# Kernel tuning notes

Hardware: AMD Instinct MI355X
Metric: run time of the kernel (lower is better)

## Reference

```python
import jax, jax.numpy as jnp
import numpy as np

B, Hc, Wc, C, NH, SR, WS = 4, 64, 64, 256, 8, 2, 4
N = Hc * Wc


def _window_partition(x, ws, H, W):
    # x: (B, h, N, d) -> (B*h*nWin, ws*ws, d)
    Bb, h, _, d = x.shape
    x = x.reshape(Bb * h, H // ws, ws, W // ws, ws, d)
    x = x.transpose(0, 1, 3, 2, 4, 5)
    return x.reshape(-1, ws * ws, d)


def _window_reverse(win, ws, H, W, head):
    nwin = (H // ws) * (W // ws)
    Bh = win.shape[0] // nwin
    x = win.reshape(Bh, H // ws, W // ws, ws, ws, -1).transpose(0, 1, 3, 2, 4, 5).reshape(Bh, H, W, -1)
    Bb = Bh // head
    x = x.reshape(Bb, head, H, W, -1).transpose(0, 2, 3, 1, 4)  # heads interleave into channels
    return x.reshape(Bb, H * W, -1)


def _layernorm(x, w, b):
    m = x.mean(-1, keepdims=True)
    v = x.var(-1, keepdims=True)
    return (x - m) / jnp.sqrt(v + 1e-5) * w + b


def setup_inputs() -> dict:
    key = jax.random.key(0)
    ks = jax.random.split(key, 16)
    lin = lambda k, i, o: 0.02 * jax.random.normal(k, (i, o), jnp.float32)
    inp = {
        'x': jax.random.normal(ks[0], (B, N, C), jnp.float32),
        'q1_w': lin(ks[1], C, C // 2), 'q1_b': jnp.zeros((C // 2,), jnp.float32),
        'kv1_w': lin(ks[2], C, C), 'kv1_b': jnp.zeros((C,), jnp.float32),
        'q2_w': lin(ks[3], C, C // 2), 'q2_b': jnp.zeros((C // 2,), jnp.float32),
        'kv2_w': lin(ks[4], C, C), 'kv2_b': jnp.zeros((C,), jnp.float32),
        'lepe_w': lin(ks[5], C, C), 'lepe_b': jnp.zeros((C,), jnp.float32),
        'lepe_conv_w': jnp.sqrt(2.0 / 9.0) * jax.random.normal(ks[6], (C, 1, 3, 3), jnp.float32),
        'lepe_conv_b': jnp.zeros((C,), jnp.float32),
        'sr_w': jnp.sqrt(2.0 / (SR * SR * C)) * jax.random.normal(ks[7], (C, C, SR, SR), jnp.float32),
        'sr_b': jnp.zeros((C,), jnp.float32),
        'norm_w': jnp.ones((C,), jnp.float32), 'norm_b': jnp.zeros((C,), jnp.float32),
        'proj_w': lin(ks[8], C, C), 'proj_b': jnp.zeros((C,), jnp.float32),
        'H': Hc, 'W': Wc,
    }
    return inp


def reference(x, q1_w, q1_b, kv1_w, kv1_b, q2_w, q2_b, kv2_w, kv2_b,
              lepe_w, lepe_b, lepe_conv_w, lepe_conv_b, sr_w, sr_b,
              norm_w, norm_b, proj_w, proj_b, H, W):
    Bb, Nn, Cc = x.shape
    h2 = NH // 2
    d = Cc // NH
    sr = sr_w.shape[-1]
    scale = d ** -0.5
    ws = WS

    # lepe: linear -> depthwise 3x3 conv
    l = (x @ lepe_w + lepe_b).transpose(0, 2, 1).reshape(Bb, Cc, H, W)
    l = jax.lax.conv_general_dilated(l, lepe_conv_w, (1, 1), ((1, 1), (1, 1)),
                                     dimension_numbers=('NCHW', 'OIHW', 'NCHW'),
                                     feature_group_count=Cc) + lepe_conv_b[None, :, None, None]
    lepe = l.reshape(Bb, Cc, Nn).transpose(0, 2, 1)

    # branch 1: spatial-reduction global attention
    q1 = (x @ q1_w + q1_b).reshape(Bb, Nn, h2, d).transpose(0, 2, 1, 3)
    x_img = x.transpose(0, 2, 1).reshape(Bb, Cc, H, W)
    xs = jax.lax.conv_general_dilated(x_img, sr_w, (sr, sr), 'VALID',
                                      dimension_numbers=('NCHW', 'OIHW', 'NCHW')) + sr_b[None, :, None, None]
    N1 = (H // sr) * (W // sr)
    xs = xs.reshape(Bb, Cc, N1).transpose(0, 2, 1)
    xs = jax.nn.gelu(_layernorm(xs, norm_w, norm_b), approximate=False)
    kv1 = (xs @ kv1_w + kv1_b).reshape(Bb, N1, 2, h2, d).transpose(2, 0, 3, 1, 4)
    k1, v1 = kv1[0], kv1[1]
    attn1 = jax.nn.softmax(jnp.einsum('bhnd,bhmd->bhnm', q1, k1) * scale, axis=-1)
    x1 = jnp.einsum('bhnm,bhmd->bnhd', attn1, v1).reshape(Bb, Nn, Cc // 2)
    g = jax.lax.stop_gradient(attn1).mean(1).mean(1).reshape(Bb, H // sr, W // sr)
    g = jnp.repeat(jnp.repeat(g, sr, axis=1), sr, axis=2)  # nearest upsample to (B,H,W)

    # branch 2: Swin-style windowed attention (window 4)
    q2 = (x @ q2_w + q2_b).reshape(Bb, Nn, h2, d).transpose(0, 2, 1, 3)
    kv2 = (x @ kv2_w + kv2_b).reshape(Bb, Nn, 2, h2, d).transpose(2, 0, 3, 1, 4)
    k2, v2 = kv2[0], kv2[1]
    q2w = _window_partition(q2, ws, H, W)
    k2w = _window_partition(k2, ws, H, W)
    v2w = _window_partition(v2, ws, H, W)
    attn2 = jax.nn.softmax(jnp.einsum('wnd,wmd->wnm', q2w, k2w) * scale, axis=-1)
    x2 = jnp.einsum('wnm,wmd->wnd', attn2, v2w)
    x2 = _window_reverse(x2, ws, H, W, h2)
    nwin = (H // ws) * (W // ws)
    lm = jax.lax.stop_gradient(attn2).reshape(Bb, h2, nwin, ws * ws, ws * ws).mean(1).mean(2)
    lm = lm.reshape(Bb, H // ws, W // ws, ws, ws).transpose(0, 1, 3, 2, 4).reshape(Bb, H, W)

    out = jnp.concatenate([x1, x2], axis=-1)
    p = (out + lepe) @ proj_w + proj_b
    out = p + p  # proj_drop is identity at p=0.0, so x = drop(p) + p = 2p

    mask = lm + g
    mask1 = mask.reshape(Bb, H * W)
    mask2 = mask.transpose(0, 2, 1).reshape(Bb, H * W)
    return out, mask1, mask2
```

## Files before the change

### kernel.cpp

```cpp
#include <hip/hip_runtime.h>
#include <hip/hip_bf16.h>
#include <math.h>

typedef __hip_bfloat16 bf16;
typedef __attribute__((ext_vector_type(8))) short bf16x8;
typedef __attribute__((ext_vector_type(4))) short bf16x4;
typedef __attribute__((ext_vector_type(4))) float f32x4;

__device__ __forceinline__ float b2f(bf16 v) { return __bfloat162float(v); }
__device__ __forceinline__ bf16  f2b(float v) { return __float2bfloat16(v); }
__device__ __forceinline__ float s2f(short v) { return __uint_as_float(((unsigned)(unsigned short)v) << 16); }

__global__ void detect_dtype(const void* x, int* flag)
{
    __shared__ int cnt;
    if (threadIdx.x == 0) cnt = 0;
    __syncthreads();
    const unsigned* w = (const unsigned*)x;
    int sane = 0;
    for (int i = threadIdx.x; i < 2048; i += 256) {
        unsigned lo = (w[i] & 0xFFFFu) << 16;
        float v = __uint_as_float(lo);
        float a = fabsf(v);
        if (v == 0.f || (a > 1e-8f && a < 1e4f)) sane++;
    }
    atomicAdd(&cnt, sane);
    __syncthreads();
    if (threadIdx.x == 0) *flag = (cnt < 1640) ? 1 : 0;
}

__global__ void convert_x4(const void* __restrict__ src, bf16* __restrict__ dst,
                           const int* __restrict__ flag)
{
    int i = blockIdx.x * 256 + threadIdx.x;
    bf16 tmp[4];
    if (*flag) {
        float4 v = ((const float4*)src)[i];
        tmp[0] = f2b(v.x); tmp[1] = f2b(v.y); tmp[2] = f2b(v.z); tmp[3] = f2b(v.w);
        *(bf16x4*)&dst[i * 4] = *(bf16x4*)tmp;
    } else {
        ((bf16x4*)dst)[i] = ((const bf16x4*)src)[i];
    }
}

struct PackArgs { const void* src[10]; bf16* dst[10]; int n[10]; };
__global__ void pack_small(PackArgs a, const int* __restrict__ flag)
{
    int bi = blockIdx.x;
    int n = a.n[bi];
    const void* s = a.src[bi];
    bf16* d = a.dst[bi];
    for (int i = threadIdx.x; i < n; i += 256)
        d[i] = (*flag) ? f2b(((const float*)s)[i]) : f2b(s2f(((const short*)s)[i]));
}

struct WTArgs { const void* src[6]; bf16* dst[6]; int N[6]; int blkoff[7]; };
__global__ void convert_wT_multi(WTArgs a, const int* __restrict__ flag)
{
    int blk = blockIdx.x;
    int ti = 0;
    while (blk >= a.blkoff[ti + 1]) ++ti;
    int o = (blk - a.blkoff[ti]) * 256 + threadIdx.x;
    int n = o >> 8, k = o & 255;
    int N = a.N[ti];
    float v = (*flag) ? ((const float*)a.src[ti])[k * N + n]
                      : s2f(((const short*)a.src[ti])[k * N + n]);
    a.dst[ti][o] = f2b(v);
}

__global__ void convert_srwT(const void* __restrict__ src, bf16* __restrict__ dst,
                             const int* __restrict__ flag)
{
    int o = blockIdx.x * 256 + threadIdx.x;
    int co = o >> 10, kg = o & 1023;
    int e = kg >> 8, ci = kg & 255;
    int si = co * 1024 + ci * 4 + e;
    float v = (*flag) ? ((const float*)src)[si] : s2f(((const short*)src)[si]);
    dst[o] = f2b(v);
}

__global__ void convert_dwT(const void* __restrict__ src, bf16* __restrict__ dst,
                            const int* __restrict__ flag)
{
    int o = blockIdx.x * 256 + threadIdx.x;
    if (o >= 2304) return;
    int k = o >> 8, c = o & 255;
    float v = (*flag) ? ((const float*)src)[c * 9 + k] : s2f(((const short*)src)[c * 9 + k]);
    dst[o] = f2b(v);
}

__global__ __launch_bounds__(256) void gemm_qkv(
    const bf16* __restrict__ A, const bf16* __restrict__ WT, const bf16* __restrict__ bias,
    bf16* __restrict__ Cl, bf16* __restrict__ Cq1, bf16* __restrict__ Cq2, bf16* __restrict__ Ckv2)
{
    __shared__ bf16 As[64][40];
    __shared__ bf16 Bs[64][40];
    int t = threadIdx.x;
    int m0 = blockIdx.x * 64, n0g = blockIdx.y * 64;
    int w = t >> 6, l = t & 63, lane16 = l & 15, quad = l >> 4;
    int sr = t >> 2, sc = (t & 3) * 8;
    f32x4 acc[4] = {};
    for (int k0 = 0; k0 < 256; k0 += 32) {
        *(bf16x8*)&As[sr][sc] = *(const bf16x8*)&A[(size_t)(m0 + sr) * 256 + k0 + sc];
        *(bf16x8*)&Bs[sr][sc] = *(const bf16x8*)&WT[(size_t)(n0g + sr) * 256 + k0 + sc];
        __syncthreads();
        bf16x8 a = *(const bf16x8*)&As[w * 16 + lane16][quad * 8];
        #pragma unroll
        for (int ct = 0; ct < 4; ++ct) {
            bf16x8 b = *(const bf16x8*)&Bs[ct * 16 + lane16][quad * 8];
            acc[ct] = __builtin_amdgcn_mfma_f32_16x16x32_bf16(a, b, acc[ct], 0, 0, 0);
        }
        __syncthreads();
    }
    bf16* C; int base, N;
    if (n0g < 256)      { C = Cl;   base = 0;   N = 256; }
    else if (n0g < 384) { C = Cq1;  base = 256; N = 128; }
    else if (n0g < 512) { C = Cq2;  base = 384; N = 128; }
    else                { C = Ckv2; base = 512; N = 256; }
    #pragma unroll
    for (int ct = 0; ct < 4; ++ct) {
        int colg = n0g + ct * 16 + lane16;
        float bv = b2f(bias[colg]);
        #pragma unroll
        for (int r = 0; r < 4; ++r) {
            int row = m0 + w * 16 + quad * 4 + r;
            C[(size_t)row * N + (colg - base)] = f2b(acc[ct][r] + bv);
        }
    }
}

__global__ __launch_bounds__(256) void gemm_sr_mfma(
    const bf16* __restrict__ x, const bf16* __restrict__ WT,
    const bf16* __restrict__ bias, bf16* __restrict__ C)
{
    __shared__ bf16 As[64][40];
    __shared__ bf16 Bs[64][40];
    int t = threadIdx.x;
    int m0 = blockIdx.x * 64, n0 = blockIdx.y * 64;
    int w = t >> 6, l = t & 63, lane16 = l & 15, quad = l >> 4;
    int sr = t >> 2, sc = (t & 3) * 8;
    int brow = m0 + sr;
    int b = brow >> 10, p = brow & 1023;
    int pi = p >> 5, pj = p & 31;
    f32x4 acc[4] = {};
    for (int k0 = 0; k0 < 1024; k0 += 32) {
        int kg = k0 + sc;
        int e = kg >> 8, ci = kg & 255;
        int di = e >> 1, dj = e & 1;
        int n = (2 * pi + di) * 64 + 2 * pj + dj;
        *(bf16x8*)&As[sr][sc] = *(const bf16x8*)&x[(size_t)((b << 12) + n) * 256 + ci];
        *(bf16x8*)&Bs[sr][sc] = *(const bf16x8*)&WT[(size_t)(n0 + sr) * 1024 + kg];
        __syncthreads();
        bf16x8 a = *(const bf16x8*)&As[w * 16 + lane16][quad * 8];
        #pragma unroll
        for (int ct = 0; ct < 4; ++ct) {
            bf16x8 bb = *(const bf16x8*)&Bs[ct * 16 + lane16][quad * 8];
            acc[ct] = __builtin_amdgcn_mfma_f32_16x16x32_bf16(a, bb, acc[ct], 0, 0, 0);
        }
        __syncthreads();
    }
    #pragma unroll
    for (int ct = 0; ct < 4; ++ct) {
        int col = n0 + ct * 16 + lane16;
        float bv = b2f(bias[col]);
        #pragma unroll
        for (int r = 0; r < 4; ++r) {
            int row = m0 + w * 16 + quad * 4 + r;
            C[(size_t)row * 256 + col] = f2b(acc[ct][r] + bv);
        }
    }
}

__global__ __launch_bounds__(256) void gemm_kv1(
    const bf16* __restrict__ A, const bf16* __restrict__ WT, const bf16* __restrict__ bias,
    bf16* __restrict__ k1, bf16* __restrict__ v1T)
{
    __shared__ bf16 As[64][40];
    __shared__ bf16 Bs[64][40];
    int t = threadIdx.x;
    int m0 = blockIdx.x * 64, n0 = blockIdx.y * 64;
    int w = t >> 6, l = t & 63, lane16 = l & 15, quad = l >> 4;
    int sr = t >> 2, sc = (t & 3) * 8;
    f32x4 acc[4] = {};
    for (int k0 = 0; k0 < 256; k0 += 32) {
        *(bf16x8*)&As[sr][sc] = *(const bf16x8*)&A[(size_t)(m0 + sr) * 256 + k0 + sc];
        *(bf16x8*)&Bs[sr][sc] = *(const bf16x8*)&WT[(size_t)(n0 + sr) * 256 + k0 + sc];
        __syncthreads();
        bf16x8 a = *(const bf16x8*)&As[w * 16 + lane16][quad * 8];
        #pragma unroll
        for (int ct = 0; ct < 4; ++ct) {
            bf16x8 b = *(const bf16x8*)&Bs[ct * 16 + lane16][quad * 8];
            acc[ct] = __builtin_amdgcn_mfma_f32_16x16x32_bf16(a, b, acc[ct], 0, 0, 0);
        }
        __syncthreads();
    }
    #pragma unroll
    for (int ct = 0; ct < 4; ++ct) {
        int col = n0 + ct * 16 + lane16;
        float bv = b2f(bias[col]);
        #pragma unroll
        for (int r = 0; r < 4; ++r) {
            int row = m0 + w * 16 + quad * 4 + r;
            float val = acc[ct][r] + bv;
            int bb = row >> 10, key = row & 1023;
            if (col < 128) {
                k1[(size_t)row * 128 + col] = f2b(val);
            } else {
                int h = (col - 128) >> 5, ch = (col - 128) & 31;
                v1T[(size_t)((bb * 4 + h) * 32 + ch) * 1024 + key] = f2b(val);
            }
        }
    }
}

__global__ __launch_bounds__(256) void gemm_proj_mfma(
    const bf16* __restrict__ A, const bf16* __restrict__ A2,
    const bf16* __restrict__ WT, const bf16* __restrict__ bias,
    void* __restrict__ dout, const int* __restrict__ flag)
{
    __shared__ bf16 As[64][40];
    __shared__ bf16 Bs[64][40];
    int t = threadIdx.x;
    int m0 = blockIdx.x * 64, n0 = blockIdx.y * 64;
    int w = t >> 6, l = t & 63, lane16 = l & 15, quad = l >> 4;
    int sr = t >> 2, sc = (t & 3) * 8;
    f32x4 acc[4] = {};
    for (int k0 = 0; k0 < 256; k0 += 32) {
        const bf16* pa = &A[(size_t)(m0 + sr) * 256 + k0 + sc];
        const bf16* pb = &A2[(size_t)(m0 + sr) * 256 + k0 + sc];
        bf16 tmp[8];
        #pragma unroll
        for (int j = 0; j < 8; ++j) tmp[j] = f2b(b2f(pa[j]) + b2f(pb[j]));
        *(bf16x8*)&As[sr][sc] = *(bf16x8*)tmp;
        *(bf16x8*)&Bs[sr][sc] = *(const bf16x8*)&WT[(size_t)(n0 + sr) * 256 + k0 + sc];
        __syncthreads();
        bf16x8 a = *(const bf16x8*)&As[w * 16 + lane16][quad * 8];
        #pragma unroll
        for (int ct = 0; ct < 4; ++ct) {
            bf16x8 b = *(const bf16x8*)&Bs[ct * 16 + lane16][quad * 8];
            acc[ct] = __builtin_amdgcn_mfma_f32_16x16x32_bf16(a, b, acc[ct], 0, 0, 0);
        }
        __syncthreads();
    }
    #pragma unroll
    for (int ct = 0; ct < 4; ++ct) {
        int col = n0 + ct * 16 + lane16;
        float bv = b2f(bias[col]);
        #pragma unroll
        for (int r = 0; r < 4; ++r) {
            int row = m0 + w * 16 + quad * 4 + r;
            float rv = (acc[ct][r] + bv) * 2.f;
            size_t o = (size_t)row * 256 + col;
            if (*flag) ((float*)dout)[o] = rv;
            else       ((bf16*)dout)[o] = f2b(rv);
        }
    }
}

__global__ __launch_bounds__(256) void dwconv3v(
    const bf16* __restrict__ lin, const bf16* __restrict__ dwT,
    const bf16* __restrict__ bias, bf16* __restrict__ out)
{
    int tid = blockIdx.x * 256 + threadIdx.x;
    int c0 = (tid & 31) * 8;
    int n = (tid >> 5) & 4095;
    int b = tid >> 17;
    int i = n >> 6, j = n & 63;
    float acc[8];
    bf16x8 bv = *(const bf16x8*)&bias[c0];
    #pragma unroll
    for (int q = 0; q < 8; ++q) acc[q] = s2f(bv[q]);
    #pragma unroll
    for (int di = 0; di < 3; ++di) {
        int ii = i + di - 1;
        if (ii < 0 || ii > 63) continue;
        #pragma unroll
        for (int dj = 0; dj < 3; ++dj) {
            int jj = j + dj - 1;
            if (jj < 0 || jj > 63) continue;
            bf16x8 xv = *(const bf16x8*)&lin[(size_t)((b << 12) + ii * 64 + jj) * 256 + c0];
            bf16x8 wv = *(const bf16x8*)&dwT[(di * 3 + dj) * 256 + c0];
            #pragma unroll
            for (int q = 0; q < 8; ++q) acc[q] += s2f(xv[q]) * s2f(wv[q]);
        }
    }
    bf16 ov[8];
    #pragma unroll
    for (int q = 0; q < 8; ++q) ov[q] = f2b(acc[q]);
    *(bf16x8*)&out[(size_t)((b << 12) + n) * 256 + c0] = *(bf16x8*)ov;
}

__global__ __launch_bounds__(256) void ln_gelu_w(
    const bf16* __restrict__ xin, const bf16* __restrict__ nw,
    const bf16* __restrict__ nb, bf16* __restrict__ xout)
{
    int w = threadIdx.x >> 6, lane = threadIdx.x & 63;
    int r = blockIdx.x * 4 + w;
    bf16x4 xv = *(const bf16x4*)&xin[(size_t)r * 256 + lane * 4];
    float v[4];
    #pragma unroll
    for (int j = 0; j < 4; ++j) v[j] = s2f(xv[j]);
    float s = v[0] + v[1] + v[2] + v[3];
    #pragma unroll
    for (int o = 1; o <= 32; o <<= 1) s += __shfl_xor(s, o);
    float mean = s * (1.f / 256.f);
    float ss = 0.f;
    #pragma unroll
    for (int j = 0; j < 4; ++j) { float d = v[j] - mean; ss += d * d; }
    #pragma unroll
    for (int o = 1; o <= 32; o <<= 1) ss += __shfl_xor(ss, o);
    float inv = rsqrtf(ss * (1.f / 256.f) + 1e-5f);
    bf16x4 wv = *(const bf16x4*)&nw[lane * 4];
    bf16x4 bv = *(const bf16x4*)&nb[lane * 4];
    bf16 ov[4];
    #pragma unroll
    for (int j = 0; j < 4; ++j) {
        float y = (v[j] - mean) * inv * s2f(wv[j]) + s2f(bv[j]);
        ov[j] = f2b(0.5f * y * (1.f + erff(y * 0.70710678118654752f)));
    }
    *(bf16x4*)&xout[(size_t)r * 256 + lane * 4] = *(bf16x4*)ov;
}

__global__ __launch_bounds__(256) void attn1_mfma2(
    const bf16* __restrict__ q1, const bf16* __restrict__ k1,
    const bf16* __restrict__ v1T, bf16* __restrict__ attn_out, float* __restrict__ g)
{
    __shared__ bf16 Kt[64][40];
    __shared__ bf16 Vt[32][68];
    __shared__ bf16 Pw[4][16][72];
    __shared__ float gp[1024];

    int t = threadIdx.x;
    int blk = blockIdx.x;
    int qc = blk & 63, h = (blk >> 6) & 3, b = blk >> 8;
    int n0 = qc * 64;
    int w = t >> 6, l = t & 63, lane16 = l & 15, quad = l >> 4;
    int sr = t >> 2, sc = (t & 3) * 8;
    const float scale = 0.17677669529663687f;

    bf16x8 qa = *(const bf16x8*)&q1[(size_t)(b * 4096 + n0 + 16 * w + lane16) * 128 + 32 * h + quad * 8];
    const bf16* Kbase = k1 + (size_t)b * 1024 * 128 + 32 * h;
    const bf16* Vbase = v1T + (size_t)((b * 4 + h) * 32) * 1024;

    for (int i = t; i < 1024; i += 256) gp[i] = 0.f;

    float lacc[4] = {0.f, 0.f, 0.f, 0.f};
    for (int kt = 0; kt < 16; ++kt) {
        *(bf16x8*)&Kt[sr][sc] = *(const bf16x8*)&Kbase[(size_t)(kt * 64 + sr) * 128 + sc];
        __syncthreads();
        #pragma unroll
        for (int st = 0; st < 4; ++st) {
            bf16x8 kb = *(const bf16x8*)&Kt[st * 16 + lane16][quad * 8];
            f32x4 z = {0.f, 0.f, 0.f, 0.f};
            f32x4 s = __builtin_amdgcn_mfma_f32_16x16x32_bf16(qa, kb, z, 0, 0, 0);
            #pragma unroll
            for (int r = 0; r < 4; ++r) lacc[r] += __expf(s[r] * scale);
        }
        __syncthreads();
    }
    float rl[4];
    #pragma unroll
    for (int r = 0; r < 4; ++r) {
        float v = lacc[r];
        v += __shfl_xor(v, 1); v += __shfl_xor(v, 2);
        v += __shfl_xor(v, 4); v += __shfl_xor(v, 8);
        rl[r] = 1.f / v;
    }

    f32x4 oacc0 = {}, oacc1 = {};
    int vrow = t >> 3, vcol = (t & 7) * 8;
    for (int kt = 0; kt < 16; ++kt) {
        *(bf16x8*)&Kt[sr][sc] = *(const bf16x8*)&Kbase[(size_t)(kt * 64 + sr) * 128 + sc];
        *(bf16x8*)&Vt[vrow][vcol] = *(const bf16x8*)&Vbase[(size_t)vrow * 1024 + kt * 64 + vcol];
        __syncthreads();
        #pragma unroll
        for (int st = 0; st < 4; ++st) {
            bf16x8 kb = *(const bf16x8*)&Kt[st * 16 + lane16][quad * 8];
            f32x4 z = {0.f, 0.f, 0.f, 0.f};
            f32x4 s = __builtin_amdgcn_mfma_f32_16x16x32_bf16(qa, kb, z, 0, 0, 0);
            float cs = 0.f;
            #pragma unroll
            for (int r = 0; r < 4; ++r) {
                float p = __expf(s[r] * scale) * rl[r];
                Pw[w][quad * 4 + r][st * 16 + lane16] = f2b(p);
                cs += p;
            }
            cs += __shfl_xor(cs, 16);
            cs += __shfl_xor(cs, 32);
            if (quad == 0) atomicAdd(&gp[kt * 64 + st * 16 + lane16], cs);
        }
        #pragma unroll
        for (int kh = 0; kh < 2; ++kh) {
            bf16x8 pa = *(const bf16x8*)&Pw[w][lane16][kh * 32 + quad * 8];
            bf16x8 vb0 = *(const bf16x8*)&Vt[lane16][kh * 32 + quad * 8];
            bf16x8 vb1 = *(const bf16x8*)&Vt[16 + lane16][kh * 32 + quad * 8];
            oacc0 = __builtin_amdgcn_mfma_f32_16x16x32_bf16(pa, vb0, oacc0, 0, 0, 0);
            oacc1 = __builtin_amdgcn_mfma_f32_16x16x32_bf16(pa, vb1, oacc1, 0, 0, 0);
        }
        __syncthreads();
    }

    #pragma unroll
    for (int r = 0; r < 4; ++r) {
        size_t ro = (size_t)(b * 4096 + n0 + 16 * w + quad * 4 + r) * 256 + 32 * h;
        attn_out[ro + lane16] = f2b(oacc0[r]);
        attn_out[ro + 16 + lane16] = f2b(oacc1[r]);
    }
    for (int i = t; i < 1024; i += 256)
        atomicAdd(&g[(b << 10) + i], gp[i] * (1.f / 16384.f));
}

__global__ __launch_bounds__(64) void attn2_vec(
    const bf16* __restrict__ q2, const bf16* __restrict__ kv2,
    bf16* __restrict__ attn_out, float* __restrict__ lm)
{
    __shared__ float P2[64][17];
    int t = threadIdx.x;
    int blk = blockIdx.x;
    int b = blk >> 8, win = blk & 255;
    int wi = win >> 4, wj = win & 15;
    int h = t >> 4, qi = t & 15;
    int nq = (wi * 4 + (qi >> 2)) * 64 + wj * 4 + (qi & 3);

    float qv[32];
    {
        const bf16* qp = q2 + (size_t)(b * 4096 + nq) * 128 + h * 32;
        #pragma unroll
        for (int g8 = 0; g8 < 4; ++g8) {
            bf16x8 v = *(const bf16x8*)&qp[g8 * 8];
            #pragma unroll
            for (int j = 0; j < 8; ++j) qv[g8 * 8 + j] = s2f(v[j]) * 0.17677669529663687f;
        }
    }
    float s[16];
    float mx = -1e30f;
    #pragma unroll
    for (int k = 0; k < 16; ++k) {
        int nk = (wi * 4 + (k >> 2)) * 64 + wj * 4 + (k & 3);
        const bf16* kp = kv2 + (size_t)(b * 4096 + nk) * 256 + h * 32;
        float ss = 0.f;
        #pragma unroll
        for (int g8 = 0; g8 < 4; ++g8) {
            bf16x8 v = *(const bf16x8*)&kp[g8 * 8];
            #pragma unroll
            for (int j = 0; j < 8; ++j) ss += qv[g8 * 8 + j] * s2f(v[j]);
        }
        s[k] = ss;
        mx = fmaxf(mx, ss);
    }
    float lsum = 0.f;
    #pragma unroll
    for (int k = 0; k < 16; ++k) { s[k] = __expf(s[k] - mx); lsum += s[k]; }
    float rl = 1.f / lsum;
    #pragma unroll
    for (int k = 0; k < 16; ++k) s[k] *= rl;

    float o[32];
    #pragma unroll
    for (int d = 0; d < 32; ++d) o[d] = 0.f;
    #pragma unroll
    for (int k = 0; k < 16; ++k) {
        int nk = (wi * 4 + (k >> 2)) * 64 + wj * 4 + (k & 3);
        const bf16* vp = kv2 + (size_t)(b * 4096 + nk) * 256 + 128 + h * 32;
        float p = s[k];
        #pragma unroll
        for (int g8 = 0; g8 < 4; ++g8) {
            bf16x8 v = *(const bf16x8*)&vp[g8 * 8];
            #pragma unroll
            for (int j = 0; j < 8; ++j) o[g8 * 8 + j] += p * s2f(v[j]);
        }
    }
    {
        bf16* op = attn_out + (size_t)(b * 4096 + nq) * 256 + 128 + h * 32;
        #pragma unroll
        for (int g8 = 0; g8 < 4; ++g8) {
            bf16 ov[8];
            #pragma unroll
            for (int j = 0; j < 8; ++j) ov[j] = f2b(o[g8 * 8 + j]);
            *(bf16x8*)&op[g8 * 8] = *(bf16x8*)ov;
        }
    }

    #pragma unroll
    for (int k = 0; k < 16; ++k) P2[t][k] = s[k];
    __syncthreads();
    if (t < 16) {
        float cs = 0.f;
        for (int qq = 0; qq < 64; ++qq) cs += P2[qq][t];
        int nk = (wi * 4 + (t >> 2)) * 64 + wj * 4 + (t & 3);
        lm[(b << 12) + nk] = cs * (1.f / 64.f);
    }
}

__global__ void mask_combine(const float* __restrict__ lm, const float* __restrict__ g,
                             void* __restrict__ dout, const int* __restrict__ flag)
{
    int tid = blockIdx.x * 256 + threadIdx.x;
    int b = tid >> 12, n = tid & 4095;
    int i = n >> 6, j = n & 63;
    float v = lm[tid] + g[(b << 10) + (i >> 1) * 32 + (j >> 1)];
    size_t o1 = (size_t)4194304 + (b << 12) + i * 64 + j;
    size_t o2 = (size_t)4194304 + 16384 + (b << 12) + j * 64 + i;
    if (*flag) { ((float*)dout)[o1] = v; ((float*)dout)[o2] = v; }
    else       { ((bf16*)dout)[o1] = f2b(v); ((bf16*)dout)[o2] = f2b(v); }
}

extern "C" void kernel_launch(void* const* d_in, const int* in_sizes, int n_in,
                              void* d_out, int out_size, void* d_ws, size_t ws_size,
                              hipStream_t stream)
{
    char* ws = (char*)d_ws;
    size_t off = 0;
    auto alloc = [&](size_t bytes) {
        void* p = ws + off;
        off += (bytes + 255) & ~(size_t)255;
        return p;
    };
    bf16* cx       = (bf16*)alloc((size_t)4194304 * 2);
    bf16* lepe_lin = (bf16*)alloc((size_t)4194304 * 2);
    bf16* attn_out = lepe_lin;
    bf16* lepe     = (bf16*)alloc((size_t)4194304 * 2);
    bf16* q1buf    = (bf16*)alloc((size_t)2097152 * 2);
    bf16* q2buf    = (bf16*)alloc((size_t)2097152 * 2);
    bf16* kv2buf   = (bf16*)alloc((size_t)4194304 * 2);
    bf16* xs_pre   = (bf16*)alloc((size_t)1048576 * 2);
    bf16* k1buf    = xs_pre;
    bf16* v1Tbuf   = xs_pre + 524288;
    bf16* xs       = (bf16*)alloc((size_t)1048576 * 2);
    bf16* wTqkv    = (bf16*)alloc((size_t)196608 * 2);
    bf16* kv1_wT   = (bf16*)alloc(65536 * 2);
    bf16* proj_wT  = (bf16*)alloc(65536 * 2);
    bf16* sr_wT    = (bf16*)alloc(262144 * 2);
    bf16* dwT      = (bf16*)alloc(2304 * 2);
    bf16* bcat     = (bf16*)alloc(768 * 2);
    bf16* ckv1b    = (bf16*)alloc(256 * 2);
    bf16* csrb     = (bf16*)alloc(256 * 2);
    bf16* cnw      = (bf16*)alloc(256 * 2);
    bf16* cnb      = (bf16*)alloc(256 * 2);
    bf16* cpb      = (bf16*)alloc(256 * 2);
    bf16* clcb     = (bf16*)alloc(256 * 2);
    float* gbuf    = (float*)alloc(4096 * 4);
    float* lmbuf   = (float*)alloc(16384 * 4);
    int*   flag    = (int*)alloc(256);

    detect_dtype<<<1, 256, 0, stream>>>(d_in[0], flag);

    convert_x4<<<4096, 256, 0, stream>>>(d_in[0], cx, flag);

    PackArgs pa;
    pa.src[0] = d_in[10]; pa.dst[0] = bcat;       pa.n[0] = 256;
    pa.src[1] = d_in[2];  pa.dst[1] = bcat + 256; pa.n[1] = 128;
    pa.src[2] = d_in[6];  pa.dst[2] = bcat + 384; pa.n[2] = 128;
    pa.src[3] = d_in[8];  pa.dst[3] = bcat + 512; pa.n[3] = 256;
    pa.src[4] = d_in[4];  pa.dst[4] = ckv1b;      pa.n[4] = 256;
    pa.src[5] = d_in[14]; pa.dst[5] = csrb;       pa.n[5] = 256;
    pa.src[6] = d_in[15]; pa.dst[6] = cnw;        pa.n[6] = 256;
    pa.src[7] = d_in[16]; pa.dst[7] = cnb;        pa.n[7] = 256;
    pa.src[8] = d_in[18]; pa.dst[8] = cpb;        pa.n[8] = 256;
    pa.src[9] = d_in[12]; pa.dst[9] = clcb;       pa.n[9] = 256;
    pack_small<<<10, 256, 0, stream>>>(pa, flag);

    WTArgs wa;
    wa.src[0] = d_in[9];  wa.dst[0] = wTqkv;             wa.N[0] = 256;
    wa.src[1] = d_in[1];  wa.dst[1] = wTqkv + 256 * 256; wa.N[1] = 128;
    wa.src[2] = d_in[5];  wa.dst[2] = wTqkv + 384 * 256; wa.N[2] = 128;
    wa.src[3] = d_in[7];  wa.dst[3] = wTqkv + 512 * 256; wa.N[3] = 256;
    wa.src[4] = d_in[3];  wa.dst[4] = kv1_wT;            wa.N[4] = 256;
    wa.src[5] = d_in[17]; wa.dst[5] = proj_wT;           wa.N[5] = 256;
    int bo[7] = {0, 256, 384, 512, 768, 1024, 1280};
    for (int i = 0; i < 7; ++i) wa.blkoff[i] = bo[i];
    convert_wT_multi<<<1280, 256, 0, stream>>>(wa, flag);

    convert_srwT<<<1024, 256, 0, stream>>>(d_in[13], sr_wT, flag);
    convert_dwT<<<9, 256, 0, stream>>>(d_in[11], dwT, flag);

    hipMemsetAsync(gbuf, 0, 4096 * 4, stream);

    gemm_qkv<<<dim3(256, 12), 256, 0, stream>>>(cx, wTqkv, bcat, lepe_lin, q1buf, q2buf, kv2buf);
    gemm_sr_mfma<<<dim3(64, 4), 256, 0, stream>>>(cx, sr_wT, csrb, xs_pre);
    ln_gelu_w<<<1024, 256, 0, stream>>>(xs_pre, cnw, cnb, xs);
    gemm_kv1<<<dim3(64, 4), 256, 0, stream>>>(xs, kv1_wT, ckv1b, k1buf, v1Tbuf);
    dwconv3v<<<2048, 256, 0, stream>>>(lepe_lin, dwT, clcb, lepe);
    attn1_mfma2<<<1024, 256, 0, stream>>>(q1buf, k1buf, v1Tbuf, attn_out, gbuf);
    attn2_vec<<<1024, 64, 0, stream>>>(q2buf, kv2buf, attn_out, lmbuf);
    gemm_proj_mfma<<<dim3(256, 4), 256, 0, stream>>>(attn_out, lepe, proj_wT, cpb, d_out, flag);
    mask_combine<<<64, 256, 0, stream>>>(lmbuf, gbuf, d_out, flag);
}
```

Measured before the change: 277.7 us.

## Use 128x128 GEMM tiles and restructure attention-1 into single-pass transposed PV

The QKV and projection GEMMs move from 64x64 to 128x128 block tiles, with each wave computing a 4x4 grid of MFMA tiles. This gives more register-level reuse per LDS load at the cost of more accumulator registers and fewer blocks. The global attention kernel now accumulates unnormalised P·V in the first pass with transposed MFMAs and normalises at the end, so the second pass only computes the mask column sums. It also drops the shared K/V staging and per-tile block barriers in favour of direct global loads into registers, which risks less coalesced access.

```diff
diff --git a/kernel.cpp b/kernel.cpp
--- a/kernel.cpp
+++ b/kernel.cpp
@@ -89,43 +89,110 @@
     dst[o] = f2b(v);
 }
 
-__global__ __launch_bounds__(256) void gemm_qkv(
+__global__ __launch_bounds__(256) void gemm_qkv128(
     const bf16* __restrict__ A, const bf16* __restrict__ WT, const bf16* __restrict__ bias,
     bf16* __restrict__ Cl, bf16* __restrict__ Cq1, bf16* __restrict__ Cq2, bf16* __restrict__ Ckv2)
 {
-    __shared__ bf16 As[64][40];
-    __shared__ bf16 Bs[64][40];
+    __shared__ bf16 As[128][40];
+    __shared__ bf16 Bs[128][40];
     int t = threadIdx.x;
-    int m0 = blockIdx.x * 64, n0g = blockIdx.y * 64;
+    int m0 = blockIdx.x * 128, ybase = blockIdx.y * 128;
     int w = t >> 6, l = t & 63, lane16 = l & 15, quad = l >> 4;
-    int sr = t >> 2, sc = (t & 3) * 8;
-    f32x4 acc[4] = {};
+    int wr = w >> 1, wc = w & 1;
+    int sr = t >> 1, sc = (t & 1) * 16;
+    f32x4 acc[4][4] = {};
     for (int k0 = 0; k0 < 256; k0 += 32) {
-        *(bf16x8*)&As[sr][sc] = *(const bf16x8*)&A[(size_t)(m0 + sr) * 256 + k0 + sc];
-        *(bf16x8*)&Bs[sr][sc] = *(const bf16x8*)&WT[(size_t)(n0g + sr) * 256 + k0 + sc];
-        __syncthreads();
-        bf16x8 a = *(const bf16x8*)&As[w * 16 + lane16][quad * 8];
-        #pragma unroll
-        for (int ct = 0; ct < 4; ++ct) {
-            bf16x8 b = *(const bf16x8*)&Bs[ct * 16 + lane16][quad * 8];
-            acc[ct] = __builtin_amdgcn_mfma_f32_16x16x32_bf16(a, b, acc[ct], 0, 0, 0);
-        }
-        __syncthreads();
-    }
-    bf16* C; int base, N;
-    if (n0g < 256)      { C = Cl;   base = 0;   N = 256; }
-    else if (n0g < 384) { C = Cq1;  base = 256; N = 128; }
-    else if (n0g < 512) { C = Cq2;  base = 384; N = 128; }
-    else                { C = Ckv2; base = 512; N = 256; }
-    #pragma unroll
-    for (int ct = 0; ct < 4; ++ct) {
-        int colg = n0g + ct * 16 + lane16;
-        float bv = b2f(bias[colg]);
-        #pragma unroll
-        for (int r = 0; r < 4; ++r) {
-            int row = m0 + w * 16 + quad * 4 + r;
-            C[(size_t)row * N + (colg - base)] = f2b(acc[ct][r] + bv);
-        }
+        *(bf16x8*)&As[sr][sc]     = *(const bf16x8*)&A[(size_t)(m0 + sr) * 256 + k0 + sc];
+        *(bf16x8*)&As[sr][sc + 8] = *(const bf16x8*)&A[(size_t)(m0 + sr) * 256 + k0 + sc + 8];
+        *(bf16x8*)&Bs[sr][sc]     = *(const bf16x8*)&WT[(size_t)(ybase + sr) * 256 + k0 + sc];
+        *(bf16x8*)&Bs[sr][sc + 8] = *(const bf16x8*)&WT[(size_t)(ybase + sr) * 256 + k0 + sc + 8];
+        __syncthreads();
+        bf16x8 a[4], b[4];
+        #pragma unroll
+        for (int i = 0; i < 4; ++i) {
+            a[i] = *(const bf16x8*)&As[wr * 64 + i * 16 + lane16][quad * 8];
+            b[i] = *(const bf16x8*)&Bs[wc * 64 + i * 16 + lane16][quad * 8];
+        }
+        #pragma unroll
+        for (int i = 0; i < 4; ++i)
+            #pragma unroll
+            for (int j = 0; j < 4; ++j)
+                acc[i][j] = __builtin_amdgcn_mfma_f32_16x16x32_bf16(a[i], b[j], acc[i][j], 0, 0, 0);
+        __syncthreads();
+    }
+    bf16* C; int N, cbase;
+    if (ybase < 256)      { C = Cl;   N = 256; cbase = ybase; }
+    else if (ybase < 384) { C = Cq1;  N = 128; cbase = ybase - 256; }
+    else if (ybase < 512) { C = Cq2;  N = 128; cbase = ybase - 384; }
+    else                  { C = Ckv2; N = 256; cbase = ybase - 512; }
+    #pragma unroll
+    for (int j = 0; j < 4; ++j) {
+        int gcol = ybase + wc * 64 + j * 16 + lane16;
+        float bv = b2f(bias[gcol]);
+        int col = cbase + wc * 64 + j * 16 + lane16;
+        #pragma unroll
+        for (int i = 0; i < 4; ++i)
+            #pragma unroll
+            for (int r = 0; r < 4; ++r) {
+                int row = m0 + wr * 64 + i * 16 + quad * 4 + r;
+                C[(size_t)row * N + col] = f2b(acc[i][j][r] + bv);
+            }
+    }
+}
+
+__global__ __launch_bounds__(256) void gemm_proj128(
+    const bf16* __restrict__ A, const bf16* __restrict__ A2,
+    const bf16* __restrict__ WT, const bf16* __restrict__ bias,
+    void* __restrict__ dout, const int* __restrict__ flag)
+{
+    __shared__ bf16 As[128][40];
+    __shared__ bf16 Bs[128][40];
+    int t = threadIdx.x;
+    int m0 = blockIdx.x * 128, n0 = blockIdx.y * 128;
+    int w = t >> 6, l = t & 63, lane16 = l & 15, quad = l >> 4;
+    int wr = w >> 1, wc = w & 1;
+    int sr = t >> 1, sc = (t & 1) * 16;
+    f32x4 acc[4][4] = {};
+    for (int k0 = 0; k0 < 256; k0 += 32) {
+        #pragma unroll
+        for (int hh = 0; hh < 2; ++hh) {
+            bf16x8 va = *(const bf16x8*)&A[(size_t)(m0 + sr) * 256 + k0 + sc + hh * 8];
+            bf16x8 vb = *(const bf16x8*)&A2[(size_t)(m0 + sr) * 256 + k0 + sc + hh * 8];
+            bf16 tmp[8];
+            #pragma unroll
+            for (int q = 0; q < 8; ++q) tmp[q] = f2b(s2f(va[q]) + s2f(vb[q]));
+            *(bf16x8*)&As[sr][sc + hh * 8] = *(bf16x8*)tmp;
+        }
+        *(bf16x8*)&Bs[sr][sc]     = *(const bf16x8*)&WT[(size_t)(n0 + sr) * 256 + k0 + sc];
+        *(bf16x8*)&Bs[sr][sc + 8] = *(const bf16x8*)&WT[(size_t)(n0 + sr) * 256 + k0 + sc + 8];
+        __syncthreads();
+        bf16x8 a[4], b[4];
+        #pragma unroll
+        for (int i = 0; i < 4; ++i) {
+            a[i] = *(const bf16x8*)&As[wr * 64 + i * 16 + lane16][quad * 8];
+            b[i] = *(const bf16x8*)&Bs[wc * 64 + i * 16 + lane16][quad * 8];
+        }
+        #pragma unroll
+        for (int i = 0; i < 4; ++i)
+            #pragma unroll
+            for (int j = 0; j < 4; ++j)
+                acc[i][j] = __builtin_amdgcn_mfma_f32_16x16x32_bf16(a[i], b[j], acc[i][j], 0, 0, 0);
+        __syncthreads();
+    }
+    #pragma unroll
+    for (int j = 0; j < 4; ++j) {
+        int col = n0 + wc * 64 + j * 16 + lane16;
+        float bv = b2f(bias[col]);
+        #pragma unroll
+        for (int i = 0; i < 4; ++i)
+            #pragma unroll
+            for (int r = 0; r < 4; ++r) {
+                int row = m0 + wr * 64 + i * 16 + quad * 4 + r;
+                float rv = (acc[i][j][r] + bv) * 2.f;
+                size_t o = (size_t)row * 256 + col;
+                if (*flag) ((float*)dout)[o] = rv;
+                else       ((bf16*)dout)[o] = f2b(rv);
+            }
     }
 }
 
@@ -213,50 +280,6 @@
     }
 }
 
-__global__ __launch_bounds__(256) void gemm_proj_mfma(
-    const bf16* __restrict__ A, const bf16* __restrict__ A2,
-    const bf16* __restrict__ WT, const bf16* __restrict__ bias,
-    void* __restrict__ dout, const int* __restrict__ flag)
-{
-    __shared__ bf16 As[64][40];
-    __shared__ bf16 Bs[64][40];
-    int t = threadIdx.x;
-    int m0 = blockIdx.x * 64, n0 = blockIdx.y * 64;
-    int w = t >> 6, l = t & 63, lane16 = l & 15, quad = l >> 4;
-    int sr = t >> 2, sc = (t & 3) * 8;
-    f32x4 acc[4] = {};
-    for (int k0 = 0; k0 < 256; k0 += 32) {
-        const bf16* pa = &A[(size_t)(m0 + sr) * 256 + k0 + sc];
-        const bf16* pb = &A2[(size_t)(m0 + sr) * 256 + k0 + sc];
-        bf16 tmp[8];
-        #pragma unroll
-        for (int j = 0; j < 8; ++j) tmp[j] = f2b(b2f(pa[j]) + b2f(pb[j]));
-        *(bf16x8*)&As[sr][sc] = *(bf16x8*)tmp;
-        *(bf16x8*)&Bs[sr][sc] = *(const bf16x8*)&WT[(size_t)(n0 + sr) * 256 + k0 + sc];
-        __syncthreads();
-        bf16x8 a = *(const bf16x8*)&As[w * 16 + lane16][quad * 8];
-        #pragma unroll
-        for (int ct = 0; ct < 4; ++ct) {
-            bf16x8 b = *(const bf16x8*)&Bs[ct * 16 + lane16][quad * 8];
-            acc[ct] = __builtin_amdgcn_mfma_f32_16x16x32_bf16(a, b, acc[ct], 0, 0, 0);
-        }
-        __syncthreads();
-    }
-    #pragma unroll
-    for (int ct = 0; ct < 4; ++ct) {
-        int col = n0 + ct * 16 + lane16;
-        float bv = b2f(bias[col]);
-        #pragma unroll
-        for (int r = 0; r < 4; ++r) {
-            int row = m0 + w * 16 + quad * 4 + r;
-            float rv = (acc[ct][r] + bv) * 2.f;
-            size_t o = (size_t)row * 256 + col;
-            if (*flag) ((float*)dout)[o] = rv;
-            else       ((bf16*)dout)[o] = f2b(rv);
-        }
-    }
-}
-
 __global__ __launch_bounds__(256) void dwconv3v(
     const bf16* __restrict__ lin, const bf16* __restrict__ dwT,
     const bf16* __restrict__ bias, bf16* __restrict__ out)
@@ -321,13 +344,11 @@
     *(bf16x4*)&xout[(size_t)r * 256 + lane * 4] = *(bf16x4*)ov;
 }
 
-__global__ __launch_bounds__(256) void attn1_mfma2(
+__global__ __launch_bounds__(256) void attn1_mfma3(
     const bf16* __restrict__ q1, const bf16* __restrict__ k1,
     const bf16* __restrict__ v1T, bf16* __restrict__ attn_out, float* __restrict__ g)
 {
-    __shared__ bf16 Kt[64][40];
-    __shared__ bf16 Vt[32][68];
-    __shared__ bf16 Pw[4][16][72];
+    __shared__ bf16 PTT[4][16][72];
     __shared__ float gp[1024];
 
     int t = threadIdx.x;
@@ -335,77 +356,81 @@
     int qc = blk & 63, h = (blk >> 6) & 3, b = blk >> 8;
     int n0 = qc * 64;
     int w = t >> 6, l = t & 63, lane16 = l & 15, quad = l >> 4;
-    int sr = t >> 2, sc = (t & 3) * 8;
     const float scale = 0.17677669529663687f;
 
-    bf16x8 qa = *(const bf16x8*)&q1[(size_t)(b * 4096 + n0 + 16 * w + lane16) * 128 + 32 * h + quad * 8];
     const bf16* Kbase = k1 + (size_t)b * 1024 * 128 + 32 * h;
     const bf16* Vbase = v1T + (size_t)((b * 4 + h) * 32) * 1024;
+    bf16x8 qa = *(const bf16x8*)&q1[(size_t)(b * 4096 + n0 + 16 * w + lane16) * 128 + 32 * h + quad * 8];
 
     for (int i = t; i < 1024; i += 256) gp[i] = 0.f;
-
-    float lacc[4] = {0.f, 0.f, 0.f, 0.f};
+    __syncthreads();
+
+    bf16* ptt = &PTT[w][0][0];
+    float lacc = 0.f;
+    f32x4 oT0 = {}, oT1 = {};
+
     for (int kt = 0; kt < 16; ++kt) {
-        *(bf16x8*)&Kt[sr][sc] = *(const bf16x8*)&Kbase[(size_t)(kt * 64 + sr) * 128 + sc];
-        __syncthreads();
+        bf16x8 kf[4];
+        #pragma unroll
+        for (int st = 0; st < 4; ++st)
+            kf[st] = *(const bf16x8*)&Kbase[(size_t)(kt * 64 + st * 16 + lane16) * 128 + quad * 8];
+        bf16x8 vf[2][2];
+        #pragma unroll
+        for (int ct = 0; ct < 2; ++ct)
+            #pragma unroll
+            for (int kh = 0; kh < 2; ++kh)
+                vf[ct][kh] = *(const bf16x8*)&Vbase[(size_t)(ct * 16 + lane16) * 1024 + kt * 64 + kh * 32 + quad * 8];
         #pragma unroll
         for (int st = 0; st < 4; ++st) {
-            bf16x8 kb = *(const bf16x8*)&Kt[st * 16 + lane16][quad * 8];
             f32x4 z = {0.f, 0.f, 0.f, 0.f};
-            f32x4 s = __builtin_amdgcn_mfma_f32_16x16x32_bf16(qa, kb, z, 0, 0, 0);
-            #pragma unroll
-            for (int r = 0; r < 4; ++r) lacc[r] += __expf(s[r] * scale);
-        }
-        __syncthreads();
-    }
-    float rl[4];
-    #pragma unroll
-    for (int r = 0; r < 4; ++r) {
-        float v = lacc[r];
-        v += __shfl_xor(v, 1); v += __shfl_xor(v, 2);
-        v += __shfl_xor(v, 4); v += __shfl_xor(v, 8);
-        rl[r] = 1.f / v;
-    }
-
-    f32x4 oacc0 = {}, oacc1 = {};
-    int vrow = t >> 3, vcol = (t & 7) * 8;
+            f32x4 sT = __builtin_amdgcn_mfma_f32_16x16x32_bf16(kf[st], qa, z, 0, 0, 0);
+            bf16 pk[4];
+            #pragma unroll
+            for (int r = 0; r < 4; ++r) {
+                float p = __expf(sT[r] * scale);
+                lacc += p;
+                pk[r] = f2b(p);
+            }
+            *(bf16x4*)&ptt[lane16 * 72 + st * 16 + quad * 4] = *(bf16x4*)pk;
+        }
+        #pragma unroll
+        for (int kh = 0; kh < 2; ++kh) {
+            bf16x8 pf = *(const bf16x8*)&ptt[lane16 * 72 + kh * 32 + quad * 8];
+            oT0 = __builtin_amdgcn_mfma_f32_16x16x32_bf16(vf[0][kh], pf, oT0, 0, 0, 0);
+            oT1 = __builtin_amdgcn_mfma_f32_16x16x32_bf16(vf[1][kh], pf, oT1, 0, 0, 0);
+        }
+    }
+    lacc += __shfl_xor(lacc, 16);
+    lacc += __shfl_xor(lacc, 32);
+    float rl = 1.f / lacc;
+    float rlq[4];
+    #pragma unroll
+    for (int r = 0; r < 4; ++r) rlq[r] = __shfl(rl, quad * 4 + r);
+
     for (int kt = 0; kt < 16; ++kt) {
-        *(bf16x8*)&Kt[sr][sc] = *(const bf16x8*)&Kbase[(size_t)(kt * 64 + sr) * 128 + sc];
-        *(bf16x8*)&Vt[vrow][vcol] = *(const bf16x8*)&Vbase[(size_t)vrow * 1024 + kt * 64 + vcol];
-        __syncthreads();
         #pragma unroll
         for (int st = 0; st < 4; ++st) {
-            bf16x8 kb = *(const bf16x8*)&Kt[st * 16 + lane16][quad * 8];
+            bf16x8 kf = *(const bf16x8*)&Kbase[(size_t)(kt * 64 + st * 16 + lane16) * 128 + quad * 8];
             f32x4 z = {0.f, 0.f, 0.f, 0.f};
-            f32x4 s = __builtin_amdgcn_mfma_f32_16x16x32_bf16(qa, kb, z, 0, 0, 0);
+            f32x4 s = __builtin_amdgcn_mfma_f32_16x16x32_bf16(qa, kf, z, 0, 0, 0);
             float cs = 0.f;
             #pragma unroll
-            for (int r = 0; r < 4; ++r) {
-                float p = __expf(s[r] * scale) * rl[r];
-                Pw[w][quad * 4 + r][st * 16 + lane16] = f2b(p);
-                cs += p;
-            }
+            for (int r = 0; r < 4; ++r) cs += __expf(s[r] * scale) * rlq[r];
             cs += __shfl_xor(cs, 16);
             cs += __shfl_xor(cs, 32);
             if (quad == 0) atomicAdd(&gp[kt * 64 + st * 16 + lane16], cs);
         }
-        #pragma unroll
-        for (int kh = 0; kh < 2; ++kh) {
-            bf16x8 pa = *(const bf16x8*)&Pw[w][lane16][kh * 32 + quad * 8];
-            bf16x8 vb0 = *(const bf16x8*)&Vt[lane16][kh * 32 + quad * 8];
-            bf16x8 vb1 = *(const bf16x8*)&Vt[16 + lane16][kh * 32 + quad * 8];
-            oacc0 = __builtin_amdgcn_mfma_f32_16x16x32_bf16(pa, vb0, oacc0, 0, 0, 0);
-            oacc1 = __builtin_amdgcn_mfma_f32_16x16x32_bf16(pa, vb1, oacc1, 0, 0, 0);
-        }
-        __syncthreads();
-    }
-
-    #pragma unroll
-    for (int r = 0; r < 4; ++r) {
-        size_t ro = (size_t)(b * 4096 + n0 + 16 * w + quad * 4 + r) * 256 + 32 * h;
-        attn_out[ro + lane16] = f2b(oacc0[r]);
-        attn_out[ro + 16 + lane16] = f2b(oacc1[r]);
-    }
+    }
+
+    #pragma unroll
+    for (int ct = 0; ct < 2; ++ct) {
+        f32x4 o = ct ? oT1 : oT0;
+        bf16 ov[4];
+        #pragma unroll
+        for (int r = 0; r < 4; ++r) ov[r] = f2b(o[r] * rl);
+        *(bf16x4*)&attn_out[(size_t)(b * 4096 + n0 + 16 * w + lane16) * 256 + 32 * h + ct * 16 + quad * 4] = *(bf16x4*)ov;
+    }
+    __syncthreads();
     for (int i = t; i < 1024; i += 256)
         atomicAdd(&g[(b << 10) + i], gp[i] * (1.f / 16384.f));
 }
@@ -576,13 +601,13 @@
 
     hipMemsetAsync(gbuf, 0, 4096 * 4, stream);
 
-    gemm_qkv<<<dim3(256, 12), 256, 0, stream>>>(cx, wTqkv, bcat, lepe_lin, q1buf, q2buf, kv2buf);
+    gemm_qkv128<<<dim3(128, 6), 256, 0, stream>>>(cx, wTqkv, bcat, lepe_lin, q1buf, q2buf, kv2buf);
     gemm_sr_mfma<<<dim3(64, 4), 256, 0, stream>>>(cx, sr_wT, csrb, xs_pre);
     ln_gelu_w<<<1024, 256, 0, stream>>>(xs_pre, cnw, cnb, xs);
     gemm_kv1<<<dim3(64, 4), 256, 0, stream>>>(xs, kv1_wT, ckv1b, k1buf, v1Tbuf);
     dwconv3v<<<2048, 256, 0, stream>>>(lepe_lin, dwT, clcb, lepe);
-    attn1_mfma2<<<1024, 256, 0, stream>>>(q1buf, k1buf, v1Tbuf, attn_out, gbuf);
+    attn1_mfma3<<<1024, 256, 0, stream>>>(q1buf, k1buf, v1Tbuf, attn_out, gbuf);
     attn2_vec<<<1024, 64, 0, stream>>>(q2buf, kv2buf, attn_out, lmbuf);
-    gemm_proj_mfma<<<dim3(256, 4), 256, 0, stream>>>(attn_out, lepe, proj_wT, cpb, d_out, flag);
+    gemm_proj128<<<dim3(128, 2), 256, 0, stream>>>(attn_out, lepe, proj_wT, cpb, d_out, flag);
     mask_combine<<<64, 256, 0, stream>>>(lmbuf, gbuf, d_out, flag);
 }
```

Result: slower. 297.9 us (+7.3%).
